# Performance work log

Hardware: AMD Instinct MI355X
Metric: run time of the kernel (lower is better)

Reference implementation:

```python
import jax, jax.numpy as jnp
import numpy as np

B, S, T = 256, 1024, 128
SOS, EOS, PAD = 0, 1, 2
NEG = -10000.0


def setup_inputs() -> dict:
    key = jax.random.key(0)
    k1, k2, k3 = jax.random.split(key, 3)
    h = jax.random.normal(k1, (B, S, T), dtype=jnp.float32)
    # realistic variable-length sequences -> float mask used in arithmetic blending
    lengths = jax.random.randint(k2, (B,), S // 2, S + 1)
    mask = (jnp.arange(S)[None, :] < lengths[:, None]).astype(jnp.float32)
    # transition matrix with the same special-tag constraints as the torch __init__
    trans = jax.random.normal(k3, (T, T), dtype=jnp.float32)
    trans = trans.at[SOS, :].set(NEG)
    trans = trans.at[:, EOS].set(NEG)
    trans = trans.at[:, PAD].set(NEG)
    trans = trans.at[PAD, :].set(NEG)
    trans = trans.at[PAD, EOS].set(0.0)
    trans = trans.at[PAD, PAD].set(0.0)
    return {"h": h, "mask": mask, "trans": trans}


def reference(h, mask, trans):
    # CRF forward (log partition function), vectorized over batch, scan over time.
    Bs, Ss, Ts = h.shape
    score0 = jnp.full((Bs, Ts), NEG, dtype=h.dtype).at[:, SOS].set(0.0)

    def step(score, xs):
        h_t, m_t = xs                      # [B,T], [B]
        # score_t[b,i,j] = score[b,j] + h[b,t,i] + trans[i,j]
        x = score[:, None, :] + h_t[:, :, None] + trans[None, :, :]  # [B,T,T]
        new = jax.nn.logsumexp(x, axis=-1)                            # [B,T]
        m = m_t[:, None]
        return new * m + score * (1.0 - m), None

    score, _ = jax.lax.scan(step, score0, (jnp.swapaxes(h, 0, 1), mask.T))
    return jax.nn.logsumexp(score + trans[EOS], axis=-1)  # [B]
```

## Files before the change

### kernel.cpp

```cpp
#include <hip/hip_runtime.h>


typedef _Float16 h2 __attribute__((ext_vector_type(2)));

static constexpr int BB = 256, SS = 1024, TT = 128, HCH = 8;
#define NEGV (-10000.0f)

__device__ __forceinline__ float dot2f(h2 a, h2 b, float c) {
    return __builtin_amdgcn_fdot2(a, b, c, false);
}

__device__ __forceinline__ float wave_max_dpp(float v) {
    int x, y;
    x = __builtin_bit_cast(int, v);
    y = __builtin_amdgcn_update_dpp(x, x, 0xB1, 0xF, 0xF, false);
    v = fmaxf(v, __builtin_bit_cast(float, y));
    x = __builtin_bit_cast(int, v);
    y = __builtin_amdgcn_update_dpp(x, x, 0x4E, 0xF, 0xF, false);
    v = fmaxf(v, __builtin_bit_cast(float, y));
    x = __builtin_bit_cast(int, v);
    y = __builtin_amdgcn_update_dpp(x, x, 0x141, 0xF, 0xF, false);
    v = fmaxf(v, __builtin_bit_cast(float, y));
    x = __builtin_bit_cast(int, v);
    y = __builtin_amdgcn_update_dpp(x, x, 0x140, 0xF, 0xF, false);
    v = fmaxf(v, __builtin_bit_cast(float, y));
    x = __builtin_bit_cast(int, v);
    y = __builtin_amdgcn_update_dpp(x, x, 0x142, 0xA, 0xF, false);
    v = fmaxf(v, __builtin_bit_cast(float, y));
    x = __builtin_bit_cast(int, v);
    y = __builtin_amdgcn_update_dpp(x, x, 0x143, 0xC, 0xF, false);
    v = fmaxf(v, __builtin_bit_cast(float, y));
    return __builtin_bit_cast(float,
        __builtin_amdgcn_readlane(__builtin_bit_cast(int, v), 63));
}

__global__ __launch_bounds__(64, 1) void crf_wave_kernel(
        const float* __restrict__ h, const float* __restrict__ mask,
        const float* __restrict__ trans, float* __restrict__ out) {
    const int b = blockIdx.x;
    const int l = threadIdx.x;
    const int i0 = 2 * l, i1 = i0 + 1;

    __shared__ alignas(16) unsigned p2[2][64];

    h2 E0[64], E1[64];
    {
        const float4* r0 = reinterpret_cast<const float4*>(trans + (size_t)i0 * TT);
        const float4* r1 = reinterpret_cast<const float4*>(trans + (size_t)i1 * TT);
        #pragma unroll
        for (int q = 0; q < 32; ++q) {
            float4 a = r0[q], c = r1[q];
            E0[2*q]   = h2{(_Float16)__expf(a.x), (_Float16)__expf(a.y)};
            E0[2*q+1] = h2{(_Float16)__expf(a.z), (_Float16)__expf(a.w)};
            E1[2*q]   = h2{(_Float16)__expf(c.x), (_Float16)__expf(c.y)};
            E1[2*q+1] = h2{(_Float16)__expf(c.z), (_Float16)__expf(c.w)};
        }
    }

    const float* mrow = mask + (size_t)b * SS;
    float cnt = 0.f;
    #pragma unroll
    for (int t = 0; t < SS / 64; ++t) cnt += mrow[t * 64 + l];
    #pragma unroll
    for (int o = 32; o; o >>= 1) cnt += __shfl_xor(cnt, o, 64);
    const int len = (int)(cnt + 0.5f);

    float s0 = (l == 0) ? 0.0f : NEGV;
    float s1 = NEGV;
    const float* hb = h + ((size_t)b * SS) * TT + i0;

    auto load_chunk = [&](float2* buf, int tbase) {
        #pragma unroll
        for (int k = 0; k < HCH; ++k) {
            int t = tbase + k; t = (t < SS) ? t : (SS - 1);
            buf[k] = *reinterpret_cast<const float2*>(hb + (size_t)t * TT);
        }
    };

    auto step = [&](float2 hk, int t) {
        const float m = wave_max_dpp(fmaxf(s0, s1));
        h2 pp = h2{(_Float16)__expf(s0 - m), (_Float16)__expf(s1 - m)};
        const int buf = t & 1;
        p2[buf][l] = __builtin_bit_cast(unsigned, pp);
        asm volatile("" ::: "memory");
        const uint4* pv = reinterpret_cast<const uint4*>(p2[buf]);
        float a0=0,a1=0,a2=0,a3=0, c0=0,c1=0,c2=0,c3=0;
        #pragma unroll
        for (int q = 0; q < 16; ++q) {
            uint4 v = pv[q];
            h2 px = __builtin_bit_cast(h2, v.x);
            h2 py = __builtin_bit_cast(h2, v.y);
            h2 pz = __builtin_bit_cast(h2, v.z);
            h2 pw = __builtin_bit_cast(h2, v.w);
            a0 = dot2f(E0[4*q+0], px, a0);
            a1 = dot2f(E0[4*q+1], py, a1);
            a2 = dot2f(E0[4*q+2], pz, a2);
            a3 = dot2f(E0[4*q+3], pw, a3);
            c0 = dot2f(E1[4*q+0], px, c0);
            c1 = dot2f(E1[4*q+1], py, c1);
            c2 = dot2f(E1[4*q+2], pz, c2);
            c3 = dot2f(E1[4*q+3], pw, c3);
        }
        float ns0 = hk.x + m + __logf((a0 + a1) + (a2 + a3));
        float ns1 = hk.y + m + __logf((c0 + c1) + (c2 + c3));
        if (t < len) { s0 = ns0; s1 = ns1; }
    };

    float2 hA[HCH], hB[HCH];
    load_chunk(hA, 0);
    for (int t0 = 0; t0 < len; t0 += 2 * HCH) {
        load_chunk(hB, t0 + HCH);
        #pragma unroll
        for (int k = 0; k < HCH; ++k) step(hA[k], t0 + k);
        load_chunk(hA, t0 + 2 * HCH);
        #pragma unroll
        for (int k = 0; k < HCH; ++k) step(hB[k], t0 + HCH + k);
    }

    float v0 = s0 + trans[1 * TT + i0];
    float v1 = s1 + trans[1 * TT + i1];
    float mm = fmaxf(v0, v1);
    #pragma unroll
    for (int o = 32; o; o >>= 1) mm = fmaxf(mm, __shfl_xor(mm, o, 64));
    float e = __expf(v0 - mm) + __expf(v1 - mm);
    #pragma unroll
    for (int o = 32; o; o >>= 1) e += __shfl_xor(e, o, 64);
    if (l == 0) out[b] = mm + __logf(e);
}

extern "C" void kernel_launch(void* const* d_in, const int* in_sizes, int n_in,
                              void* d_out, int out_size, void* d_ws, size_t ws_size,
                              hipStream_t stream) {
    const float* h     = (const float*)d_in[0];
    const float* mask  = (const float*)d_in[1];
    const float* trans = (const float*)d_in[2];
    float* out         = (float*)d_out;
    crf_wave_kernel<<<dim3(BB), dim3(64), 0, stream>>>(h, mask, trans, out);
}
```

Before: 483.8 us.

## Run CRF recursion in linear domain with power-of-two rescaling

Replaces the per-step log-domain update (wave max, exp of scores, log of sums) with a linear-space recursion that multiplies by exp(h) and a deferred power-of-two scale factor derived from the wave max exponent bits. Accumulated exponents are tracked in an integer and converted back to log only at the end. This takes the max reduction and exp off the critical path before the dot products and drops the per-step log, and it uses a single LDS buffer. The cost is fp16 range/precision risk, since values are scaled by the previous step's max rather than the current one.

```diff
diff --git a/kernel.cpp b/kernel.cpp
--- a/kernel.cpp
+++ b/kernel.cpp
@@ -4,7 +4,7 @@
 typedef _Float16 h2 __attribute__((ext_vector_type(2)));
 
 static constexpr int BB = 256, SS = 1024, TT = 128, HCH = 8;
-#define NEGV (-10000.0f)
+#define LN2F 0.69314718056f
 
 __device__ __forceinline__ float dot2f(h2 a, h2 b, float c) {
     return __builtin_amdgcn_fdot2(a, b, c, false);
@@ -34,14 +34,14 @@
         __builtin_amdgcn_readlane(__builtin_bit_cast(int, v), 63));
 }
 
-__global__ __launch_bounds__(64, 1) void crf_wave_kernel(
+__global__ __launch_bounds__(64, 1) void crf_lin_kernel(
         const float* __restrict__ h, const float* __restrict__ mask,
         const float* __restrict__ trans, float* __restrict__ out) {
     const int b = blockIdx.x;
     const int l = threadIdx.x;
     const int i0 = 2 * l, i1 = i0 + 1;
 
-    __shared__ alignas(16) unsigned p2[2][64];
+    __shared__ alignas(16) unsigned V2[64];
 
     h2 E0[64], E1[64];
     {
@@ -65,8 +65,12 @@
     for (int o = 32; o; o >>= 1) cnt += __shfl_xor(cnt, o, 64);
     const int len = (int)(cnt + 0.5f);
 
-    float s0 = (l == 0) ? 0.0f : NEGV;
-    float s1 = NEGV;
+    V2[l] = (l == 0) ? 0x00002000u : 0u;
+    asm volatile("" ::: "memory");
+    int   kacc = 7;
+    float F    = 1.0f;   int e7F = 0;
+    float sv0  = (l == 0) ? 0.0078125f : 0.0f, sv1 = 0.0f;
+
     const float* hb = h + ((size_t)b * SS) * TT + i0;
 
     auto load_chunk = [&](float2* buf, int tbase) {
@@ -78,12 +82,8 @@
     };
 
     auto step = [&](float2 hk, int t) {
-        const float m = wave_max_dpp(fmaxf(s0, s1));
-        h2 pp = h2{(_Float16)__expf(s0 - m), (_Float16)__expf(s1 - m)};
-        const int buf = t & 1;
-        p2[buf][l] = __builtin_bit_cast(unsigned, pp);
-        asm volatile("" ::: "memory");
-        const uint4* pv = reinterpret_cast<const uint4*>(p2[buf]);
+        float eh0 = __expf(hk.x), eh1 = __expf(hk.y);
+        const uint4* pv = reinterpret_cast<const uint4*>(V2);
         float a0=0,a1=0,a2=0,a3=0, c0=0,c1=0,c2=0,c3=0;
         #pragma unroll
         for (int q = 0; q < 16; ++q) {
@@ -101,9 +101,20 @@
             c2 = dot2f(E1[4*q+2], pz, c2);
             c3 = dot2f(E1[4*q+3], pw, c3);
         }
-        float ns0 = hk.x + m + __logf((a0 + a1) + (a2 + a3));
-        float ns1 = hk.y + m + __logf((c0 + c1) + (c2 + c3));
-        if (t < len) { s0 = ns0; s1 = ns1; }
+        float u0 = (a0 + a1) + (a2 + a3);
+        float u1 = (c0 + c1) + (c2 + c3);
+        float V0 = u0 * eh0 * F;
+        float V1 = u1 * eh1 * F;
+        h2 pp = h2{(_Float16)V0, (_Float16)V1};
+        const bool live = (t < len);
+        if (live) V2[l] = __builtin_bit_cast(unsigned, pp);
+        asm volatile("" ::: "memory");
+        float w = wave_max_dpp(fmaxf(V0, V1));
+        unsigned wb = __builtin_bit_cast(unsigned, w);
+        int Eb  = (int)((wb >> 23) & 0xffu) + (int)((wb >> 22) & 1u);
+        int e7n = Eb - 120;
+        float Fn = __builtin_bit_cast(float, (unsigned)(127 - e7n) << 23);
+        if (live) { sv0 = V0; sv1 = V1; kacc += e7F; F = Fn; e7F = e7n; }
     };
 
     float2 hA[HCH], hB[HCH];
@@ -117,8 +128,9 @@
         for (int k = 0; k < HCH; ++k) step(hB[k], t0 + HCH + k);
     }
 
-    float v0 = s0 + trans[1 * TT + i0];
-    float v1 = s1 + trans[1 * TT + i1];
+    const float base = (float)kacc * LN2F;
+    float v0 = __logf(sv0) + base + trans[1 * TT + i0];
+    float v1 = __logf(sv1) + base + trans[1 * TT + i1];
     float mm = fmaxf(v0, v1);
     #pragma unroll
     for (int o = 32; o; o >>= 1) mm = fmaxf(mm, __shfl_xor(mm, o, 64));
@@ -135,5 +147,5 @@
     const float* mask  = (const float*)d_in[1];
     const float* trans = (const float*)d_in[2];
     float* out         = (float*)d_out;
-    crf_wave_kernel<<<dim3(BB), dim3(64), 0, stream>>>(h, mask, trans, out);
+    crf_lin_kernel<<<dim3(BB), dim3(64), 0, stream>>>(h, mask, trans, out);
 }
```

Result: slower. 501.3 us (+3.6%).
